# Optimization experiments

Hardware: AMD Instinct MI355X
Metric: run time of the kernel (lower is better)

Reference implementation:

```python
import jax, jax.numpy as jnp
import numpy as np

B, N, K = 32, 2048, 16          # graphs, nodes per graph, knn neighbors
F_IN, F_OUT, P = 32, 64, 3      # feature dims, pos dim


def setup_inputs() -> dict:
    key = jax.random.key(0)
    ks = jax.random.split(key, 6)
    x = jax.random.normal(ks[0], (B * N, F_IN), dtype=jnp.float32)
    pos = jax.random.normal(ks[1], (B * N, P), dtype=jnp.float32)
    # contiguous equal-size graphs: batch[i] = i // N
    batch = (jnp.arange(B * N, dtype=jnp.int32) // N).astype(jnp.int32)
    W_edge = jax.random.normal(ks[2], (2 * F_IN, F_OUT), dtype=jnp.float32) * 0.1
    b_edge = jax.random.normal(ks[3], (F_OUT,), dtype=jnp.float32) * 0.1
    W_nn = jax.random.normal(ks[4], (F_IN, F_OUT), dtype=jnp.float32) * 0.1
    b_nn = jax.random.normal(ks[5], (F_OUT,), dtype=jnp.float32) * 0.1
    return {"x": x, "pos": pos, "W_edge": W_edge, "b_edge": b_edge,
            "W_nn": W_nn, "b_nn": b_nn, "batch": batch}


def reference(x, pos, W_edge, b_edge, W_nn, b_nn, batch):
    # batch is contiguous with N nodes per graph -> reshape to [B, N, .]
    xb = x.reshape(B, N, F_IN)
    pb = pos.reshape(B, N, P)

    # --- knn_graph on pos, per graph (flow='source_to_target') ---
    sq = jnp.sum(pb * pb, axis=-1)                                   # [B, N]
    d2 = sq[:, :, None] + sq[:, None, :] - 2.0 * jnp.einsum('bnd,bmd->bnm', pb, pb)
    d2 = d2 + jnp.eye(N, dtype=d2.dtype) * 1e30                      # exclude self-loops
    _, idx = jax.lax.top_k(-d2, K)                                   # idx[b, i, k] = k-th nearest j of i

    # --- EdgeConv: message = edge_nn(concat(x_i, x_j - x_i)), aggr=max at i ---
    x_j = jnp.take_along_axis(xb, idx.reshape(B, N * K, 1), axis=1).reshape(B, N, K, F_IN)
    x_i = xb[:, :, None, :]                                          # [B, N, 1, F_IN]
    msg = jnp.concatenate([jnp.broadcast_to(x_i, (B, N, K, F_IN)), x_j - x_i], axis=-1)
    h = jax.nn.relu(msg @ W_edge + b_edge)                           # [B, N, K, F_OUT]
    edge_out = jnp.max(h, axis=2)                                    # max-aggregate over neighbors

    # --- skip branch: nn(x) ---
    skip = jax.nn.relu(xb @ W_nn + b_nn)                             # [B, N, F_OUT]

    return (edge_out + skip).reshape(B * N, F_OUT)
```

## Files before the change

kernel.cpp:

```cpp
#include <hip/hip_runtime.h>

#define NB     32
#define NPTS   2048
#define KNN    16
#define FIN    32
#define FOUT   64

typedef __attribute__((ext_vector_type(8))) short bf16x8;
typedef __attribute__((ext_vector_type(4))) float f32x4;

__device__ inline unsigned bf16pk(float lo, float hi) {
    unsigned a = __float_as_uint(lo), b = __float_as_uint(hi);
    a = (a + 0x7fffu + ((a >> 16) & 1u)) >> 16;
    b = (b + 0x7fffu + ((b >> 16) & 1u)) >> 16;
    return (a & 0xffffu) | (b << 16);
}


#define CEA(x, y) { float _t = fminf(x, y); y = fmaxf(x, y); x = _t; }
#define CED(x, y) { float _t = fmaxf(x, y); y = fminf(x, y); x = _t; }

#define BMERGE16(dk) \
    CEA(dk[0],dk[8])  CEA(dk[1],dk[9])  CEA(dk[2],dk[10]) CEA(dk[3],dk[11]) \
    CEA(dk[4],dk[12]) CEA(dk[5],dk[13]) CEA(dk[6],dk[14]) CEA(dk[7],dk[15]) \
    CEA(dk[0],dk[4])  CEA(dk[1],dk[5])  CEA(dk[2],dk[6])  CEA(dk[3],dk[7])  \
    CEA(dk[8],dk[12]) CEA(dk[9],dk[13]) CEA(dk[10],dk[14]) CEA(dk[11],dk[15]) \
    CEA(dk[0],dk[2])  CEA(dk[1],dk[3])  CEA(dk[4],dk[6])  CEA(dk[5],dk[7])  \
    CEA(dk[8],dk[10]) CEA(dk[9],dk[11]) CEA(dk[12],dk[14]) CEA(dk[13],dk[15]) \
    CEA(dk[0],dk[1])  CEA(dk[2],dk[3])  CEA(dk[4],dk[5])  CEA(dk[6],dk[7])  \
    CEA(dk[8],dk[9])  CEA(dk[10],dk[11]) CEA(dk[12],dk[13]) CEA(dk[14],dk[15])

__global__ __launch_bounds__(256) void sq_kernel(
    const float* __restrict__ pos, float4* __restrict__ P4)
{
    const int i = blockIdx.x * 256 + threadIdx.x;
    const float px = pos[i*3 + 0];
    const float py = pos[i*3 + 1];
    const float pz = pos[i*3 + 2];
    const float sq = __fadd_rn(__fadd_rn(__fmul_rn(px,px), __fmul_rn(py,py)),
                               __fmul_rn(pz,pz));
    P4[i] = make_float4(px, py, pz, sq);
}

#define CH   8
#define CHL  (NPTS / CH)

#define D2P(C, DST)                                                        \
    {                                                                      \
        float _dot = __fmaf_rn(me.z, (C).z,                                \
                      __fmaf_rn(me.y, (C).y, __fmul_rn(me.x, (C).x)));     \
        DST = __fmaf_rn(-2.0f, _dot, (C).w);                               \
    }

#define SBATCH(JB, EXCLF)                                                  \
    {                                                                      \
        float a[8];                                                        \
        _Pragma("unroll")                                                  \
        for (int i = 0; i < 8; ++i) {                                      \
            const int j = (JB) + i;                                        \
            const float4 c = pb4[j];                                       \
            float d2;                                                      \
            D2P(c, d2)                                                     \
            a[i] = (EXCLF && j == q) ? 1e30f : d2;                         \
        }                                                                  \
        CED(a[0],a[1]) CED(a[2],a[3]) CED(a[4],a[5]) CED(a[6],a[7])        \
        CED(a[0],a[2]) CED(a[1],a[3]) CED(a[4],a[6]) CED(a[5],a[7])        \
        CED(a[1],a[2]) CED(a[5],a[6])                                      \
        CED(a[0],a[4]) CED(a[1],a[5]) CED(a[2],a[6]) CED(a[3],a[7])        \
        CED(a[2],a[4]) CED(a[3],a[5])                                      \
        CED(a[1],a[2]) CED(a[3],a[4]) CED(a[5],a[6])                       \
        _Pragma("unroll")                                                  \
        for (int i = 0; i < 8; ++i) dk[8+i] = fminf(dk[8+i], a[i]);        \
        BMERGE16(dk)                                                       \
    }

#define APP(DD, JJ)                                                        \
    if ((DD) <= tthr) {                                                    \
        if ((DD) < tthr) {                                                 \
            if (cntS + cntT >= KNN) --cntT;                                \
            JL[base + cntS * 64 + l] = (JJ);                               \
            ++cntS;                                                        \
        } else if (cntS + cntT < KNN) {                                    \
            JL[base + (KNN - 1 - cntT) * 64 + l] = (JJ);                   \
            ++cntT;                                                        \
        }                                                                  \
    }

#define RESC(JJ, EXCLF)                                                    \
    {                                                                      \
        const float4 c = pb4[(JJ)];                                        \
        float d2;                                                          \
        D2P(c, d2)                                                         \
        if (EXCLF && (JJ) == q) d2 = 1e30f;                                \
        APP(d2, (JJ))                                                      \
    }

__global__ __launch_bounds__(512, 8) void knn_kernel(
    const float4* __restrict__ P4, int* __restrict__ idxws)
{
    __shared__ float V[CH * KNN * 64];
    __shared__ int   CNTS[CH * 64];

    const int b    = blockIdx.x >> 5;
    const int slab = blockIdx.x & 31;
    const int t    = threadIdx.x;
    const int w    = __builtin_amdgcn_readfirstlane(t >> 6);
    const int l    = t & 63;

    const float4* __restrict__ pb4 = P4 + (size_t)b * NPTS;

    const int    q  = slab * 64 + l;
    const float4 me = pb4[q];

    float dk[KNN];
    #pragma unroll
    for (int s = 0; s < KNN; ++s) dk[s] = 1e30f;

    const int j0  = w * CHL;
    const int exw = slab >> 2;
    const int lo  = j0 + (slab & 3) * 64;

    if (w == exw) {
        for (int jb = j0;      jb < lo;        jb += 8) SBATCH(jb, false)
        for (int jb = lo;      jb < lo + 64;   jb += 8) SBATCH(jb, true)
        for (int jb = lo + 64; jb < j0 + CHL;  jb += 8) SBATCH(jb, false)
    } else {
        for (int jb = j0;      jb < j0 + CHL;  jb += 8) SBATCH(jb, false)
    }

    #pragma unroll
    for (int s = 0; s < KNN; ++s)
        V[(w * KNN + s) * 64 + l] = dk[s];
    __syncthreads();

    for (int c2 = 0; c2 < CH; ++c2) {
        if (c2 == w) continue;
        float v[KNN];
        #pragma unroll
        for (int s2 = 0; s2 < KNN; ++s2)
            v[s2] = V[(c2 * KNN + s2) * 64 + l];
        #pragma unroll
        for (int s = 0; s < KNN; ++s) dk[s] = fminf(dk[s], v[KNN-1-s]);
        BMERGE16(dk)
    }
    const float tthr = dk[KNN-1];
    __syncthreads();

    int* JL = (int*)V;
    const int base = w * KNN * 64;
    int cntS = 0, cntT = 0;
    if (w == exw) {
        for (int j = j0;      j < lo;        ++j) RESC(j, false)
        for (int j = lo;      j < lo + 64;   ++j) RESC(j, true)
        for (int j = lo + 64; j < j0 + CHL;  ++j) RESC(j, false)
    } else {
        for (int j = j0;      j < j0 + CHL;  ++j) RESC(j, false)
    }
    CNTS[w * 64 + l] = cntS | (cntT << 16);
    __syncthreads();

    if (w == 0) {
        int* o = idxws + ((size_t)b * NPTS + q) * KNN;
        int outc = 0;
        for (int c2 = 0; c2 < CH; ++c2) {
            int cs = CNTS[c2 * 64 + l] & 0xffff;
            for (int s2 = 0; s2 < cs && outc < KNN; ++s2)
                o[outc++] = JL[(c2 * KNN + s2) * 64 + l];
        }
        for (int c2 = 0; c2 < CH && outc < KNN; ++c2) {
            int ct = CNTS[c2 * 64 + l] >> 16;
            for (int s2 = 0; s2 < ct && outc < KNN; ++s2)
                o[outc++] = JL[(c2 * KNN + (KNN - 1 - s2)) * 64 + l];
        }
    }
}

__global__ __launch_bounds__(512) void mlp_kernel(
    const float* __restrict__ x,
    const float* __restrict__ W_edge, const float* __restrict__ b_edge,
    const float* __restrict__ W_nn,   const float* __restrict__ b_nn,
    const int* __restrict__ idxws, float* __restrict__ out)
{
    __shared__ float Z[8 * 16 * 64];

    const int b    = blockIdx.x >> 4;
    const int qgb  = blockIdx.x & 15;
    const int t    = threadIdx.x;
    const int w    = t >> 6;
    const int lane = t & 63;
    const int c15  = lane & 15;
    const int g    = lane >> 4;

    float* Zw = Z + w * (16 * 64);

    const int n0    = b * NPTS + qgb * 128 + w * 16;
    const int gbase = b * NPTS;

    int4 Bhi[4], Bd[4], Bn[4];
    #pragma unroll
    for (int f = 0; f < 4; ++f) {
        const int col = 16 * f + c15;
        unsigned ph[4], pd[4], pn[4];
        #pragma unroll
        for (int d = 0; d < 4; ++d) {
            const int k0 = g * 8 + 2 * d;
            float h0 = W_edge[(FIN + k0)     * FOUT + col];
            float h1 = W_edge[(FIN + k0 + 1) * FOUT + col];
            float l0 = W_edge[k0       * FOUT + col] - h0;
            float l1 = W_edge[(k0 + 1) * FOUT + col] - h1;
            float n0f = W_nn[k0       * FOUT + col];
            float n1f = W_nn[(k0 + 1) * FOUT + col];
            ph[d] = bf16pk(h0, h1);
            pd[d] = bf16pk(l0, l1);
            pn[d] = bf16pk(n0f, n1f);
        }
        Bhi[f] = make_int4(ph[0], ph[1], ph[2], ph[3]);
        Bd[f]  = make_int4(pd[0], pd[1], pd[2], pd[3]);
        Bn[f]  = make_int4(pn[0], pn[1], pn[2], pn[3]);
    }
    float beF[4], bnF[4];
    #pragma unroll
    for (int f = 0; f < 4; ++f) {
        beF[f] = b_edge[16 * f + c15];
        bnF[f] = b_nn[16 * f + c15];
    }

    const f32x4 zf = {0.f, 0.f, 0.f, 0.f};

    f32x4 baseF[4], skipF[4];
    {
        const float* rp = x + (size_t)(n0 + c15) * FIN + g * 8;
        float4 v0 = *(const float4*)rp;
        float4 v1 = *(const float4*)(rp + 4);
        int4 pk = make_int4(bf16pk(v0.x, v0.y), bf16pk(v0.z, v0.w),
                            bf16pk(v1.x, v1.y), bf16pk(v1.z, v1.w));
        bf16x8 afi = *(bf16x8*)&pk;
        #pragma unroll
        for (int f = 0; f < 4; ++f) {
            baseF[f] = __builtin_amdgcn_mfma_f32_16x16x32_bf16(
                afi, *(bf16x8*)&Bd[f], zf, 0, 0, 0);
            skipF[f] = __builtin_amdgcn_mfma_f32_16x16x32_bf16(
                afi, *(bf16x8*)&Bn[f], zf, 0, 0, 0);
        }
    }

    int nb0 = idxws[(size_t)n0 * KNN + c15];
    const float* rpp = x + (size_t)(gbase + nb0) * FIN + g * 8;
    float4 pv0 = *(const float4*)rpp;
    float4 pv1 = *(const float4*)(rpp + 4);

    #pragma unroll 1
    for (int i = 0; i < 16; ++i) {
        float4 c0 = pv0, c1 = pv1;
        if (i < 15) {
            int nb = idxws[(size_t)(n0 + i + 1) * KNN + c15];
            const float* rp = x + (size_t)(gbase + nb) * FIN + g * 8;
            pv0 = *(const float4*)rp;
            pv1 = *(const float4*)(rp + 4);
        }
        int4 pk = make_int4(bf16pk(c0.x, c0.y), bf16pk(c0.z, c0.w),
                            bf16pk(c1.x, c1.y), bf16pk(c1.z, c1.w));
        bf16x8 af = *(bf16x8*)&pk;

        float rmax[4];
        #pragma unroll
        for (int f = 0; f < 4; ++f) {
            f32x4 z = __builtin_amdgcn_mfma_f32_16x16x32_bf16(
                af, *(bf16x8*)&Bhi[f], zf, 0, 0, 0);
            float m = fmaxf(fmaxf(z[0], z[1]), fmaxf(z[2], z[3]));
            m = fmaxf(m, __shfl_xor(m, 16));
            m = fmaxf(m, __shfl_xor(m, 32));
            rmax[f] = m;
        }
        float zv = (g == 0) ? rmax[0] : (g == 1) ? rmax[1]
                 : (g == 2) ? rmax[2] : rmax[3];
        Zw[i * 64 + 16 * g + c15] = zv;
    }

    #pragma unroll
    for (int f = 0; f < 4; ++f) {
        #pragma unroll
        for (int reg = 0; reg < 4; ++reg) {
            const int nd = g * 4 + reg;
            float zmax = Zw[nd * 64 + 16 * f + c15];
            float e  = fmaxf(zmax + baseF[f][reg] + beF[f], 0.f);
            float sk = fmaxf(skipF[f][reg] + bnF[f], 0.f);
            out[(size_t)(n0 + nd) * FOUT + 16 * f + c15] = e + sk;
        }
    }
}

extern "C" void kernel_launch(void* const* d_in, const int* in_sizes, int n_in,
                              void* d_out, int out_size, void* d_ws, size_t ws_size,
                              hipStream_t stream) {
    const float* x      = (const float*)d_in[0];
    const float* pos    = (const float*)d_in[1];
    const float* W_edge = (const float*)d_in[2];
    const float* b_edge = (const float*)d_in[3];
    const float* W_nn   = (const float*)d_in[4];
    const float* b_nn   = (const float*)d_in[5];

    int*    idxws = (int*)d_ws;
    float4* P4    = (float4*)((char*)d_ws + (4u << 20));
    float*  outp  = (float*)d_out;

    sq_kernel <<<NB * NPTS / 256, 256, 0, stream>>>(pos, P4);
    knn_kernel<<<NB * 32,         512, 0, stream>>>(P4, idxws);
    mlp_kernel<<<NB * 16,         512, 0, stream>>>(x, W_edge, b_edge,
                                                    W_nn, b_nn, idxws, outp);
}
```

Measured before the change: 215.1 us.

## Fuse kNN selection with EdgeConv MLP and batch 16 candidates per merge

The kNN kernel and the MLP kernel are merged into one kernel. Neighbor indices now stay in shared memory instead of going through a global workspace, and the work is split so each wave handles 16 nodes and 2 of the 4 output column groups. The candidate scan also computes 16 distances per step, as two sorted 8-wide groups, before merging them into the running top-16. This removes a kernel launch and the global index round trip, but the MLP phase now runs on the kNN kernel's 512-thread blocks of 64 nodes and repeats some weight loading per block.

```diff
diff --git a/kernel.cpp b/kernel.cpp
--- a/kernel.cpp
+++ b/kernel.cpp
@@ -29,6 +29,14 @@
     CEA(dk[8],dk[10]) CEA(dk[9],dk[11]) CEA(dk[12],dk[14]) CEA(dk[13],dk[15]) \
     CEA(dk[0],dk[1])  CEA(dk[2],dk[3])  CEA(dk[4],dk[5])  CEA(dk[6],dk[7])  \
     CEA(dk[8],dk[9])  CEA(dk[10],dk[11]) CEA(dk[12],dk[13]) CEA(dk[14],dk[15])
+
+#define NET8(a) \
+    CED(a[0],a[1]) CED(a[2],a[3]) CED(a[4],a[5]) CED(a[6],a[7]) \
+    CED(a[0],a[2]) CED(a[1],a[3]) CED(a[4],a[6]) CED(a[5],a[7]) \
+    CED(a[1],a[2]) CED(a[5],a[6]) \
+    CED(a[0],a[4]) CED(a[1],a[5]) CED(a[2],a[6]) CED(a[3],a[7]) \
+    CED(a[2],a[4]) CED(a[3],a[5]) \
+    CED(a[1],a[2]) CED(a[3],a[4]) CED(a[5],a[6])
 
 __global__ __launch_bounds__(256) void sq_kernel(
     const float* __restrict__ pos, float4* __restrict__ P4)
@@ -52,9 +60,9 @@
         DST = __fmaf_rn(-2.0f, _dot, (C).w);                               \
     }
 
-#define SBATCH(JB, EXCLF)                                                  \
+#define SBATCH2(JB, EXCLF)                                                 \
     {                                                                      \
-        float a[8];                                                        \
+        float a[8], a2[8];                                                 \
         _Pragma("unroll")                                                  \
         for (int i = 0; i < 8; ++i) {                                      \
             const int j = (JB) + i;                                        \
@@ -63,14 +71,21 @@
             D2P(c, d2)                                                     \
             a[i] = (EXCLF && j == q) ? 1e30f : d2;                         \
         }                                                                  \
-        CED(a[0],a[1]) CED(a[2],a[3]) CED(a[4],a[5]) CED(a[6],a[7])        \
-        CED(a[0],a[2]) CED(a[1],a[3]) CED(a[4],a[6]) CED(a[5],a[7])        \
-        CED(a[1],a[2]) CED(a[5],a[6])                                      \
-        CED(a[0],a[4]) CED(a[1],a[5]) CED(a[2],a[6]) CED(a[3],a[7])        \
-        CED(a[2],a[4]) CED(a[3],a[5])                                      \
-        CED(a[1],a[2]) CED(a[3],a[4]) CED(a[5],a[6])                       \
+        _Pragma("unroll")                                                  \
+        for (int i = 0; i < 8; ++i) {                                      \
+            const int j = (JB) + 8 + i;                                    \
+            const float4 c = pb4[j];                                       \
+            float d2;                                                      \
+            D2P(c, d2)                                                     \
+            a2[i] = (EXCLF && j == q) ? 1e30f : d2;                        \
+        }                                                                  \
+        NET8(a)                                                            \
+        NET8(a2)                                                           \
         _Pragma("unroll")                                                  \
         for (int i = 0; i < 8; ++i) dk[8+i] = fminf(dk[8+i], a[i]);        \
+        BMERGE16(dk)                                                       \
+        _Pragma("unroll")                                                  \
+        for (int i = 0; i < 8; ++i) dk[8+i] = fminf(dk[8+i], a2[i]);       \
         BMERGE16(dk)                                                       \
     }
 
@@ -95,11 +110,15 @@
         APP(d2, (JJ))                                                      \
     }
 
-__global__ __launch_bounds__(512, 8) void knn_kernel(
-    const float4* __restrict__ P4, int* __restrict__ idxws)
+__global__ __launch_bounds__(512, 8) void knn_mlp_kernel(
+    const float4* __restrict__ P4, const float* __restrict__ x,
+    const float* __restrict__ W_edge, const float* __restrict__ b_edge,
+    const float* __restrict__ W_nn,   const float* __restrict__ b_nn,
+    float* __restrict__ out)
 {
     __shared__ float V[CH * KNN * 64];
     __shared__ int   CNTS[CH * 64];
+    __shared__ int   IDX[64 * KNN];
 
     const int b    = blockIdx.x >> 5;
     const int slab = blockIdx.x & 31;
@@ -107,185 +126,177 @@
     const int w    = __builtin_amdgcn_readfirstlane(t >> 6);
     const int l    = t & 63;
 
-    const float4* __restrict__ pb4 = P4 + (size_t)b * NPTS;
-
-    const int    q  = slab * 64 + l;
-    const float4 me = pb4[q];
-
-    float dk[KNN];
-    #pragma unroll
-    for (int s = 0; s < KNN; ++s) dk[s] = 1e30f;
-
-    const int j0  = w * CHL;
-    const int exw = slab >> 2;
-    const int lo  = j0 + (slab & 3) * 64;
-
-    if (w == exw) {
-        for (int jb = j0;      jb < lo;        jb += 8) SBATCH(jb, false)
-        for (int jb = lo;      jb < lo + 64;   jb += 8) SBATCH(jb, true)
-        for (int jb = lo + 64; jb < j0 + CHL;  jb += 8) SBATCH(jb, false)
-    } else {
-        for (int jb = j0;      jb < j0 + CHL;  jb += 8) SBATCH(jb, false)
-    }
-
-    #pragma unroll
-    for (int s = 0; s < KNN; ++s)
-        V[(w * KNN + s) * 64 + l] = dk[s];
-    __syncthreads();
-
-    for (int c2 = 0; c2 < CH; ++c2) {
-        if (c2 == w) continue;
-        float v[KNN];
-        #pragma unroll
-        for (int s2 = 0; s2 < KNN; ++s2)
-            v[s2] = V[(c2 * KNN + s2) * 64 + l];
-        #pragma unroll
-        for (int s = 0; s < KNN; ++s) dk[s] = fminf(dk[s], v[KNN-1-s]);
-        BMERGE16(dk)
-    }
-    const float tthr = dk[KNN-1];
-    __syncthreads();
-
-    int* JL = (int*)V;
-    const int base = w * KNN * 64;
-    int cntS = 0, cntT = 0;
-    if (w == exw) {
-        for (int j = j0;      j < lo;        ++j) RESC(j, false)
-        for (int j = lo;      j < lo + 64;   ++j) RESC(j, true)
-        for (int j = lo + 64; j < j0 + CHL;  ++j) RESC(j, false)
-    } else {
-        for (int j = j0;      j < j0 + CHL;  ++j) RESC(j, false)
-    }
-    CNTS[w * 64 + l] = cntS | (cntT << 16);
-    __syncthreads();
-
-    if (w == 0) {
-        int* o = idxws + ((size_t)b * NPTS + q) * KNN;
-        int outc = 0;
+    {
+        const float4* __restrict__ pb4 = P4 + (size_t)b * NPTS;
+
+        const int    q  = slab * 64 + l;
+        const float4 me = pb4[q];
+
+        float dk[KNN];
+        #pragma unroll
+        for (int s = 0; s < KNN; ++s) dk[s] = 1e30f;
+
+        const int j0  = w * CHL;
+        const int exw = slab >> 2;
+        const int lo  = j0 + (slab & 3) * 64;
+
+        if (w == exw) {
+            for (int jb = j0;      jb < lo;        jb += 16) SBATCH2(jb, false)
+            for (int jb = lo;      jb < lo + 64;   jb += 16) SBATCH2(jb, true)
+            for (int jb = lo + 64; jb < j0 + CHL;  jb += 16) SBATCH2(jb, false)
+        } else {
+            for (int jb = j0;      jb < j0 + CHL;  jb += 16) SBATCH2(jb, false)
+        }
+
+        #pragma unroll
+        for (int s = 0; s < KNN; ++s)
+            V[(w * KNN + s) * 64 + l] = dk[s];
+        __syncthreads();
+
         for (int c2 = 0; c2 < CH; ++c2) {
-            int cs = CNTS[c2 * 64 + l] & 0xffff;
-            for (int s2 = 0; s2 < cs && outc < KNN; ++s2)
-                o[outc++] = JL[(c2 * KNN + s2) * 64 + l];
-        }
-        for (int c2 = 0; c2 < CH && outc < KNN; ++c2) {
-            int ct = CNTS[c2 * 64 + l] >> 16;
-            for (int s2 = 0; s2 < ct && outc < KNN; ++s2)
-                o[outc++] = JL[(c2 * KNN + (KNN - 1 - s2)) * 64 + l];
-        }
-    }
-}
-
-__global__ __launch_bounds__(512) void mlp_kernel(
-    const float* __restrict__ x,
-    const float* __restrict__ W_edge, const float* __restrict__ b_edge,
-    const float* __restrict__ W_nn,   const float* __restrict__ b_nn,
-    const int* __restrict__ idxws, float* __restrict__ out)
-{
-    __shared__ float Z[8 * 16 * 64];
-
-    const int b    = blockIdx.x >> 4;
-    const int qgb  = blockIdx.x & 15;
-    const int t    = threadIdx.x;
-    const int w    = t >> 6;
-    const int lane = t & 63;
-    const int c15  = lane & 15;
-    const int g    = lane >> 4;
-
-    float* Zw = Z + w * (16 * 64);
-
-    const int n0    = b * NPTS + qgb * 128 + w * 16;
-    const int gbase = b * NPTS;
-
-    int4 Bhi[4], Bd[4], Bn[4];
-    #pragma unroll
-    for (int f = 0; f < 4; ++f) {
-        const int col = 16 * f + c15;
-        unsigned ph[4], pd[4], pn[4];
-        #pragma unroll
-        for (int d = 0; d < 4; ++d) {
-            const int k0 = g * 8 + 2 * d;
-            float h0 = W_edge[(FIN + k0)     * FOUT + col];
-            float h1 = W_edge[(FIN + k0 + 1) * FOUT + col];
-            float l0 = W_edge[k0       * FOUT + col] - h0;
-            float l1 = W_edge[(k0 + 1) * FOUT + col] - h1;
-            float n0f = W_nn[k0       * FOUT + col];
-            float n1f = W_nn[(k0 + 1) * FOUT + col];
-            ph[d] = bf16pk(h0, h1);
-            pd[d] = bf16pk(l0, l1);
-            pn[d] = bf16pk(n0f, n1f);
-        }
-        Bhi[f] = make_int4(ph[0], ph[1], ph[2], ph[3]);
-        Bd[f]  = make_int4(pd[0], pd[1], pd[2], pd[3]);
-        Bn[f]  = make_int4(pn[0], pn[1], pn[2], pn[3]);
-    }
-    float beF[4], bnF[4];
-    #pragma unroll
-    for (int f = 0; f < 4; ++f) {
-        beF[f] = b_edge[16 * f + c15];
-        bnF[f] = b_nn[16 * f + c15];
-    }
-
-    const f32x4 zf = {0.f, 0.f, 0.f, 0.f};
-
-    f32x4 baseF[4], skipF[4];
+            if (c2 == w) continue;
+            float v[KNN];
+            #pragma unroll
+            for (int s2 = 0; s2 < KNN; ++s2)
+                v[s2] = V[(c2 * KNN + s2) * 64 + l];
+            #pragma unroll
+            for (int s = 0; s < KNN; ++s) dk[s] = fminf(dk[s], v[KNN-1-s]);
+            BMERGE16(dk)
+        }
+        const float tthr = dk[KNN-1];
+        __syncthreads();
+
+        int* JL = (int*)V;
+        const int base = w * KNN * 64;
+        int cntS = 0, cntT = 0;
+        if (w == exw) {
+            for (int j = j0;      j < lo;        ++j) RESC(j, false)
+            for (int j = lo;      j < lo + 64;   ++j) RESC(j, true)
+            for (int j = lo + 64; j < j0 + CHL;  ++j) RESC(j, false)
+        } else {
+            for (int j = j0;      j < j0 + CHL;  ++j) RESC(j, false)
+        }
+        CNTS[w * 64 + l] = cntS | (cntT << 16);
+        __syncthreads();
+
+        if (w == 0) {
+            int outc = 0;
+            for (int c2 = 0; c2 < CH; ++c2) {
+                int cs = CNTS[c2 * 64 + l] & 0xffff;
+                for (int s2 = 0; s2 < cs && outc < KNN; ++s2)
+                    IDX[l * KNN + outc++] = JL[(c2 * KNN + s2) * 64 + l];
+            }
+            for (int c2 = 0; c2 < CH && outc < KNN; ++c2) {
+                int ct = CNTS[c2 * 64 + l] >> 16;
+                for (int s2 = 0; s2 < ct && outc < KNN; ++s2)
+                    IDX[l * KNN + outc++] =
+                        JL[(c2 * KNN + (KNN - 1 - s2)) * 64 + l];
+            }
+        }
+        __syncthreads();
+    }
+
     {
-        const float* rp = x + (size_t)(n0 + c15) * FIN + g * 8;
-        float4 v0 = *(const float4*)rp;
-        float4 v1 = *(const float4*)(rp + 4);
-        int4 pk = make_int4(bf16pk(v0.x, v0.y), bf16pk(v0.z, v0.w),
-                            bf16pk(v1.x, v1.y), bf16pk(v1.z, v1.w));
-        bf16x8 afi = *(bf16x8*)&pk;
-        #pragma unroll
-        for (int f = 0; f < 4; ++f) {
-            baseF[f] = __builtin_amdgcn_mfma_f32_16x16x32_bf16(
-                afi, *(bf16x8*)&Bd[f], zf, 0, 0, 0);
-            skipF[f] = __builtin_amdgcn_mfma_f32_16x16x32_bf16(
-                afi, *(bf16x8*)&Bn[f], zf, 0, 0, 0);
-        }
-    }
-
-    int nb0 = idxws[(size_t)n0 * KNN + c15];
-    const float* rpp = x + (size_t)(gbase + nb0) * FIN + g * 8;
-    float4 pv0 = *(const float4*)rpp;
-    float4 pv1 = *(const float4*)(rpp + 4);
-
-    #pragma unroll 1
-    for (int i = 0; i < 16; ++i) {
-        float4 c0 = pv0, c1 = pv1;
-        if (i < 15) {
-            int nb = idxws[(size_t)(n0 + i + 1) * KNN + c15];
-            const float* rp = x + (size_t)(gbase + nb) * FIN + g * 8;
-            pv0 = *(const float4*)rp;
-            pv1 = *(const float4*)(rp + 4);
-        }
-        int4 pk = make_int4(bf16pk(c0.x, c0.y), bf16pk(c0.z, c0.w),
-                            bf16pk(c1.x, c1.y), bf16pk(c1.z, c1.w));
-        bf16x8 af = *(bf16x8*)&pk;
-
-        float rmax[4];
-        #pragma unroll
-        for (int f = 0; f < 4; ++f) {
-            f32x4 z = __builtin_amdgcn_mfma_f32_16x16x32_bf16(
-                af, *(bf16x8*)&Bhi[f], zf, 0, 0, 0);
-            float m = fmaxf(fmaxf(z[0], z[1]), fmaxf(z[2], z[3]));
-            m = fmaxf(m, __shfl_xor(m, 16));
-            m = fmaxf(m, __shfl_xor(m, 32));
-            rmax[f] = m;
-        }
-        float zv = (g == 0) ? rmax[0] : (g == 1) ? rmax[1]
-                 : (g == 2) ? rmax[2] : rmax[3];
-        Zw[i * 64 + 16 * g + c15] = zv;
-    }
-
-    #pragma unroll
-    for (int f = 0; f < 4; ++f) {
-        #pragma unroll
-        for (int reg = 0; reg < 4; ++reg) {
-            const int nd = g * 4 + reg;
-            float zmax = Zw[nd * 64 + 16 * f + c15];
-            float e  = fmaxf(zmax + baseF[f][reg] + beF[f], 0.f);
-            float sk = fmaxf(skipF[f][reg] + bnF[f], 0.f);
-            out[(size_t)(n0 + nd) * FOUT + 16 * f + c15] = e + sk;
+        const int c15 = l & 15;
+        const int g   = l >> 4;
+        const int ng  = w & 3;
+        const int f0  = (w >> 2) * 2;
+
+        float* Zw = V + ng * (16 * 64);
+
+        const int n0    = b * NPTS + slab * 64 + ng * 16;
+        const int gbase = b * NPTS;
+
+        int4 Bhi[2], Bd[2], Bn[2];
+        #pragma unroll
+        for (int ff = 0; ff < 2; ++ff) {
+            const int col = 16 * (f0 + ff) + c15;
+            unsigned ph[4], pd[4], pn[4];
+            #pragma unroll
+            for (int d = 0; d < 4; ++d) {
+                const int k0 = g * 8 + 2 * d;
+                float h0 = W_edge[(FIN + k0)     * FOUT + col];
+                float h1 = W_edge[(FIN + k0 + 1) * FOUT + col];
+                float l0 = W_edge[k0       * FOUT + col] - h0;
+                float l1 = W_edge[(k0 + 1) * FOUT + col] - h1;
+                float n0f = W_nn[k0       * FOUT + col];
+                float n1f = W_nn[(k0 + 1) * FOUT + col];
+                ph[d] = bf16pk(h0, h1);
+                pd[d] = bf16pk(l0, l1);
+                pn[d] = bf16pk(n0f, n1f);
+            }
+            Bhi[ff] = make_int4(ph[0], ph[1], ph[2], ph[3]);
+            Bd[ff]  = make_int4(pd[0], pd[1], pd[2], pd[3]);
+            Bn[ff]  = make_int4(pn[0], pn[1], pn[2], pn[3]);
+        }
+        float beF[2], bnF[2];
+        #pragma unroll
+        for (int ff = 0; ff < 2; ++ff) {
+            beF[ff] = b_edge[16 * (f0 + ff) + c15];
+            bnF[ff] = b_nn[16 * (f0 + ff) + c15];
+        }
+
+        const f32x4 zf = {0.f, 0.f, 0.f, 0.f};
+
+        f32x4 baseF[2], skipF[2];
+        {
+            const float* rp = x + (size_t)(n0 + c15) * FIN + g * 8;
+            float4 v0 = *(const float4*)rp;
+            float4 v1 = *(const float4*)(rp + 4);
+            int4 pk = make_int4(bf16pk(v0.x, v0.y), bf16pk(v0.z, v0.w),
+                                bf16pk(v1.x, v1.y), bf16pk(v1.z, v1.w));
+            bf16x8 afi = *(bf16x8*)&pk;
+            #pragma unroll
+            for (int ff = 0; ff < 2; ++ff) {
+                baseF[ff] = __builtin_amdgcn_mfma_f32_16x16x32_bf16(
+                    afi, *(bf16x8*)&Bd[ff], zf, 0, 0, 0);
+                skipF[ff] = __builtin_amdgcn_mfma_f32_16x16x32_bf16(
+                    afi, *(bf16x8*)&Bn[ff], zf, 0, 0, 0);
+            }
+        }
+
+        int nb0 = IDX[(ng * 16 + 0) * KNN + c15];
+        const float* rpp = x + (size_t)(gbase + nb0) * FIN + g * 8;
+        float4 pv0 = *(const float4*)rpp;
+        float4 pv1 = *(const float4*)(rpp + 4);
+
+        #pragma unroll 1
+        for (int i = 0; i < 16; ++i) {
+            float4 c0 = pv0, c1 = pv1;
+            if (i < 15) {
+                int nb = IDX[(ng * 16 + i + 1) * KNN + c15];
+                const float* rp = x + (size_t)(gbase + nb) * FIN + g * 8;
+                pv0 = *(const float4*)rp;
+                pv1 = *(const float4*)(rp + 4);
+            }
+            int4 pk = make_int4(bf16pk(c0.x, c0.y), bf16pk(c0.z, c0.w),
+                                bf16pk(c1.x, c1.y), bf16pk(c1.z, c1.w));
+            bf16x8 af = *(bf16x8*)&pk;
+
+            float rmax[2];
+            #pragma unroll
+            for (int ff = 0; ff < 2; ++ff) {
+                f32x4 z = __builtin_amdgcn_mfma_f32_16x16x32_bf16(
+                    af, *(bf16x8*)&Bhi[ff], zf, 0, 0, 0);
+                float m = fmaxf(fmaxf(z[0], z[1]), fmaxf(z[2], z[3]));
+                m = fmaxf(m, __shfl_xor(m, 16));
+                m = fmaxf(m, __shfl_xor(m, 32));
+                rmax[ff] = m;
+            }
+            if (g < 2)
+                Zw[i * 64 + 16 * (f0 + g) + c15] = (g == 0) ? rmax[0] : rmax[1];
+        }
+
+        #pragma unroll
+        for (int ff = 0; ff < 2; ++ff) {
+            #pragma unroll
+            for (int reg = 0; reg < 4; ++reg) {
+                const int nd = g * 4 + reg;
+                float zmax = Zw[nd * 64 + 16 * (f0 + ff) + c15];
+                float e  = fmaxf(zmax + baseF[ff][reg] + beF[ff], 0.f);
+                float sk = fmaxf(skipF[ff][reg] + bnF[ff], 0.f);
+                out[(size_t)(n0 + nd) * FOUT + 16 * (f0 + ff) + c15] = e + sk;
+            }
         }
     }
 }
@@ -300,12 +311,10 @@
     const float* W_nn   = (const float*)d_in[4];
     const float* b_nn   = (const float*)d_in[5];
 
-    int*    idxws = (int*)d_ws;
-    float4* P4    = (float4*)((char*)d_ws + (4u << 20));
-    float*  outp  = (float*)d_out;
-
-    sq_kernel <<<NB * NPTS / 256, 256, 0, stream>>>(pos, P4);
-    knn_kernel<<<NB * 32,         512, 0, stream>>>(P4, idxws);
-    mlp_kernel<<<NB * 16,         512, 0, stream>>>(x, W_edge, b_edge,
-                                                    W_nn, b_nn, idxws, outp);
+    float4* P4   = (float4*)d_ws;
+    float*  outp = (float*)d_out;
+
+    sq_kernel     <<<NB * NPTS / 256, 256, 0, stream>>>(pos, P4);
+    knn_mlp_kernel<<<NB * 32,         512, 0, stream>>>(P4, x, W_edge, b_edge,
+                                                        W_nn, b_nn, outp);
 }
```

Result: faster. 205.9 us (-4.3%).
